# Performance work log

Hardware: AMD Instinct MI355X
Metric: run time of the kernel (lower is better)

Reference implementation:

```python
import jax, jax.numpy as jnp
import numpy as np

B, CH, H, W = 32, 128, 32, 32
EMB = 64      # embedding_dim
NEMB = 8192   # codebook size


def setup_inputs() -> dict:
    key = jax.random.key(0)
    k1, k2, k3, k4 = jax.random.split(key, 4)
    z = jax.random.normal(k1, (B, CH, H, W), jnp.float32)
    # 1x1 conv == per-pixel linear: weight [EMB, CH], bias [EMB]
    proj_w = jax.random.normal(k2, (EMB, CH), jnp.float32) * 0.05
    proj_b = jax.random.normal(k3, (EMB,), jnp.float32) * 0.01
    embed_w = jax.random.normal(k4, (NEMB, EMB), jnp.float32)
    return {"z": z, "proj_w": proj_w, "proj_b": proj_b, "embed_w": embed_w}


def reference(z, proj_w, proj_b, embed_w):
    Bz, C, Hh, Ww = z.shape
    sg = jax.lax.stop_gradient
    # 1x1 conv then permute(0,2,3,1): [B,C,H,W] -> [B,H,W,E]
    z_e = jnp.einsum('bchw,ec->bhwe', z, proj_w) + proj_b
    flat = z_e.reshape(-1, z_e.shape[-1])  # [N, E], N = B*H*W
    dist = ((flat * flat).sum(1, keepdims=True)
            - 2.0 * (flat @ embed_w.T)
            + (embed_w * embed_w).sum(1)[None, :])
    z_q_ind = jnp.argmin(dist, axis=1).reshape(Bz, Hh, Ww)  # argmax(-dist)
    z_q_emb = embed_w[z_q_ind]  # gather: [B,H,W,E]
    commitment_cost = 0.25
    kld_scale = 10.0
    latent_loss = kld_scale * (
        commitment_cost * jnp.mean((sg(z_q_emb) - z_e) ** 2)
        + jnp.mean((z_q_emb - sg(z_e)) ** 2))
    z_q_flat = z_q_emb
    # straight-through estimator
    z_q_st = z_e + sg(z_q_emb - z_e)
    out = jnp.transpose(z_q_st, (0, 3, 1, 2))  # [B,E,H,W]
    return out, z_q_flat, latent_loss, z_q_ind
```

## Files before the change

kernel.cpp:

```cpp
#include <hip/hip_runtime.h>

#define NPIX   32768
#define NEMB_  8192
#define EMB_   64
#define CH_    128
#define CAPP   768

#define OUT_OFF  0
#define ZQ_OFF   2097152
#define LOSS_OFF 4194304
#define IND_OFF  4194305

typedef _Float16 h8   __attribute__((ext_vector_type(8)));
typedef float    f16f __attribute__((ext_vector_type(16)));

__global__ __launch_bounds__(64) void k_wpack(
    const float* __restrict__ ew, const float* __restrict__ pw,
    float4* __restrict__ W4, float* __restrict__ pwT,
    float* __restrict__ wsq, float* __restrict__ wsqp,
    float* __restrict__ lacc, int* __restrict__ done)
{
    const int tid = threadIdx.x;
    {
        const int i = blockIdx.x * 64 + tid;
        const float v = pw[i];
        const int e = i >> 7, c = i & 127;
        pwT[c * 64 + e] = v;
    }
    const int m = blockIdx.x * 64 + tid;
    const float4* wr = (const float4*)(ew + (size_t)m * EMB_);
    float w[EMB_];
    float s = 0.f;
    #pragma unroll
    for (int i = 0; i < 16; i++) {
        float4 v = wr[i];
        w[4*i] = v.x; w[4*i+1] = v.y; w[4*i+2] = v.z; w[4*i+3] = v.w;
        s += v.x*v.x + v.y*v.y + v.z*v.z + v.w*v.w;
    }
    wsq[m] = s;
    float sh = (float)(_Float16)s;
    float sl = s - sh;
    const int t  = m >> 5;
    const int li = m & 31;
    #pragma unroll
    for (int s5 = 0; s5 < 4; s5++) {
        #pragma unroll
        for (int h = 0; h < 2; h++) {
            h8 hh;
            #pragma unroll
            for (int j = 0; j < 8; j++) hh[j] = (_Float16)w[s5 * 16 + h * 8 + j];
            W4[(size_t)(t * 5 + s5) * 64 + h * 32 + li] = __builtin_bit_cast(float4, hh);
        }
    }
    {
        h8 hh;
        #pragma unroll
        for (int j = 0; j < 8; j++) hh[j] = (_Float16)0.f;
        hh[0] = (_Float16)sh; hh[1] = (_Float16)sl;
        W4[(size_t)(t * 5 + 4) * 64 + 0 * 32 + li] = __builtin_bit_cast(float4, hh);
        #pragma unroll
        for (int j = 0; j < 8; j++) hh[j] = (_Float16)0.f;
        W4[(size_t)(t * 5 + 4) * 64 + 1 * 32 + li] = __builtin_bit_cast(float4, hh);
    }
    float sm = s;
    #pragma unroll
    for (int o = 32; o > 0; o >>= 1) sm = fmaxf(sm, __shfl_xor(sm, o));
    if (tid == 0) wsqp[blockIdx.x] = sm;
    if (blockIdx.x == 0 && tid == 0) { *lacc = 0.f; *done = 0; }
}

__device__ __forceinline__ unsigned long long pack_key(float d, int m)
{
    unsigned fb = __float_as_uint(d);
    fb ^= ((int)fb < 0) ? 0xFFFFFFFFu : 0x80000000u;
    return ((unsigned long long)fb << 32) | (unsigned)m;
}

__global__ __launch_bounds__(1024, 4) void k_fused3(
    const float4* __restrict__ W4, const float* __restrict__ z,
    const float* __restrict__ pwT, const float* __restrict__ pb,
    const float* __restrict__ wsqp, const float* __restrict__ wsq,
    const float* __restrict__ ew,
    float* __restrict__ out, float* __restrict__ lacc, int* __restrict__ done)
{
    __shared__ __align__(16) float xs[128][68];
    __shared__ float s1s[1024], s2s[1024], s3s[1024];
    __shared__ short i1s[1024], i2s[1024];
    __shared__ float xsqp_s[8][128];
    __shared__ float thr_s[128];
    __shared__ int   pairs[CAPP];
    __shared__ unsigned long long pbest[128];
    __shared__ int   winner_s[128];
    __shared__ int   smask[128];
    __shared__ float wred[16];
    __shared__ int   npair_s;
    __shared__ float wm_s;

    const int tid  = threadIdx.x;
    const int wv   = tid >> 6;
    const int lane = tid & 63;
    const int n0   = blockIdx.x * 128;
    const int hlf  = lane >> 5;

    if (tid == 0) npair_s = 0;
    if (tid < 128) { smask[tid] = 0; pbest[tid] = ~0ULL; }
    if (tid < 64) {
        float w = fmaxf(wsqp[tid], wsqp[tid + 64]);
        #pragma unroll
        for (int o = 32; o > 0; o >>= 1) w = fmaxf(w, __shfl_xor(w, o));
        if (tid == 0) wm_s = w;
    }

    {
        const int oct = tid >> 7;
        const int pxp = tid & 127;
        const int e0  = __builtin_amdgcn_readfirstlane(oct << 3);
        const float* zp = z + (size_t)(n0 >> 10) * (CH_ * 1024) + (n0 & 1023) + pxp;
        float acc[8];
        #pragma unroll
        for (int j = 0; j < 8; j++) acc[j] = 0.f;
        #pragma unroll 8
        for (int c = 0; c < CH_; c++) {
            const float zv = zp[(size_t)c * 1024];
            const float4* wr = (const float4*)(pwT + c * 64 + e0);
            float4 w0 = wr[0], w1 = wr[1];
            acc[0] = fmaf(zv, w0.x, acc[0]); acc[1] = fmaf(zv, w0.y, acc[1]);
            acc[2] = fmaf(zv, w0.z, acc[2]); acc[3] = fmaf(zv, w0.w, acc[3]);
            acc[4] = fmaf(zv, w1.x, acc[4]); acc[5] = fmaf(zv, w1.y, acc[5]);
            acc[6] = fmaf(zv, w1.z, acc[6]); acc[7] = fmaf(zv, w1.w, acc[7]);
        }
        const float4* pb4 = (const float4*)(pb + e0);
        float4 b0 = pb4[0], b1 = pb4[1];
        acc[0] += b0.x; acc[1] += b0.y; acc[2] += b0.z; acc[3] += b0.w;
        acc[4] += b1.x; acc[5] += b1.y; acc[6] += b1.z; acc[7] += b1.w;
        float sq = 0.f;
        #pragma unroll
        for (int j = 0; j < 8; j++) sq += acc[j] * acc[j];
        ((float4*)&xs[pxp][0])[oct * 2]     = make_float4(acc[0], acc[1], acc[2], acc[3]);
        ((float4*)&xs[pxp][0])[oct * 2 + 1] = make_float4(acc[4], acc[5], acc[6], acc[7]);
        xsqp_s[oct][pxp] = sq;
    }
    __syncthreads();

    const int ch = wv & 7;
    const int pg = wv >> 3;

    h8 bfr[2][4];
    #pragma unroll
    for (int j = 0; j < 2; j++) {
        const int px = pg * 64 + j * 32 + (lane & 31);
        #pragma unroll
        for (int s5 = 0; s5 < 4; s5++) {
            float4 u0 = *(const float4*)(&xs[px][s5 * 16 + hlf * 8]);
            float4 u1 = *(const float4*)(&xs[px][s5 * 16 + hlf * 8 + 4]);
            h8 hh;
            hh[0]=(_Float16)u0.x; hh[1]=(_Float16)u0.y; hh[2]=(_Float16)u0.z; hh[3]=(_Float16)u0.w;
            hh[4]=(_Float16)u1.x; hh[5]=(_Float16)u1.y; hh[6]=(_Float16)u1.z; hh[7]=(_Float16)u1.w;
            bfr[j][s5] = hh;
        }
    }
    h8 btail;
    {
        h8 hh;
        #pragma unroll
        for (int q = 0; q < 8; q++) hh[q] = (_Float16)0.f;
        if (hlf == 0) { hh[0] = (_Float16)-0.5f; hh[1] = (_Float16)-0.5f; }
        btail = hh;
    }

    const f16f kzero = {0,0,0,0,0,0,0,0,0,0,0,0,0,0,0,0};
    float s1[2], s2[2], s3[2];
    int   i1[2], i2[2];
    #pragma unroll
    for (int j = 0; j < 2; j++) { s1[j]=s2[j]=s3[j]=-3.0e38f; i1[j]=i2[j]=0; }

    const int tb = ch * 32;
    const float4* Wb = W4 + (size_t)tb * 320 + lane;
    float4 A[5];
    #pragma unroll
    for (int s = 0; s < 5; s++) A[s] = Wb[s * 64];

#define REDUCE_J(ACC, JJ, GT)                                                  \
    {                                                                          \
        float t0 = fmaxf(fmaxf(ACC[0],  ACC[1]),  ACC[2]);                     \
        float t1 = fmaxf(fmaxf(ACC[3],  ACC[4]),  ACC[5]);                     \
        float t2 = fmaxf(fmaxf(ACC[6],  ACC[7]),  ACC[8]);                     \
        float t3 = fmaxf(fmaxf(ACC[9],  ACC[10]), ACC[11]);                    \
        float t4 = fmaxf(fmaxf(ACC[12], ACC[13]), ACC[14]);                    \
        float v  = fmaxf(fmaxf(fmaxf(t0, t1), fmaxf(t2, t3)),                  \
                         fmaxf(t4, ACC[15]));                                  \
        bool c1 = v > s1[JJ];                                                  \
        bool c2 = v > s2[JJ];                                                  \
        int  cand = c1 ? i1[JJ] : (GT);                                        \
        i2[JJ] = c2 ? cand : i2[JJ];                                           \
        s3[JJ] = fmaxf(fminf(s2[JJ], v), s3[JJ]);                              \
        s3[JJ] = fminf(s3[JJ], fmaxf(s2[JJ], v));                              \
        s2[JJ] = fmaxf(fminf(s1[JJ], v), fminf(s2[JJ], fmaxf(s1[JJ], v)));     \
        i1[JJ] = c1 ? (GT) : i1[JJ];                                           \
        s1[JJ] = fmaxf(s1[JJ], v);                                             \
    }

    for (int tt = 0; tt < 32; tt++) {
        const int gt = tb + tt;
        f16f acc0 = __builtin_amdgcn_mfma_f32_32x32x16_f16(
            __builtin_bit_cast(h8, A[0]), bfr[0][0], kzero, 0, 0, 0);
        #pragma unroll
        for (int s = 1; s < 4; s++)
            acc0 = __builtin_amdgcn_mfma_f32_32x32x16_f16(
                __builtin_bit_cast(h8, A[s]), bfr[0][s], acc0, 0, 0, 0);
        acc0 = __builtin_amdgcn_mfma_f32_32x32x16_f16(
            __builtin_bit_cast(h8, A[4]), btail, acc0, 0, 0, 0);
        REDUCE_J(acc0, 0, gt)
        f16f acc1 = __builtin_amdgcn_mfma_f32_32x32x16_f16(
            __builtin_bit_cast(h8, A[0]), bfr[1][0], kzero, 0, 0, 0);
        #pragma unroll
        for (int s = 1; s < 4; s++)
            acc1 = __builtin_amdgcn_mfma_f32_32x32x16_f16(
                __builtin_bit_cast(h8, A[s]), bfr[1][s], acc1, 0, 0, 0);
        acc1 = __builtin_amdgcn_mfma_f32_32x32x16_f16(
            __builtin_bit_cast(h8, A[4]), btail, acc1, 0, 0, 0);
        {
            const int tp = (tt + 1) < 32 ? (tt + 1) : 31;
            const float4* wp = Wb + (size_t)tp * 320;
            #pragma unroll
            for (int s = 0; s < 5; s++) A[s] = wp[s * 64];
        }
        REDUCE_J(acc1, 1, gt)
    }
#undef REDUCE_J

    #pragma unroll
    for (int j = 0; j < 2; j++) {
        const float o1 = __shfl_xor(s1[j], 32);
        const float o2 = __shfl_xor(s2[j], 32);
        const float o3 = __shfl_xor(s3[j], 32);
        const int  oi1 = __shfl_xor(i1[j], 32);
        const int  oi2 = __shfl_xor(i2[j], 32);
        const bool a1  = s1[j] >= o1;
        const float m1 = a1 ? s1[j] : o1;
        const int  mi1 = a1 ? i1[j] : oi1;
        const float hA = a1 ? s2[j] : s1[j];
        const int  hAi = a1 ? i2[j] : i1[j];
        const float hB = a1 ? o1 : o2;
        const int  hBi = a1 ? oi1 : oi2;
        const bool b2  = hA >= hB;
        const float m2 = b2 ? hA : hB;
        const int  mi2 = b2 ? hAi : hBi;
        const float nA = b2 ? (a1 ? s3[j] : s2[j]) : hA;
        const float nB = b2 ? hB : (a1 ? o2 : o3);
        const float m3 = fmaxf(nA, nB);
        s1[j] = m1; s2[j] = m2; s3[j] = m3; i1[j] = mi1; i2[j] = mi2;
    }

    if (lane < 32) {
        #pragma unroll
        for (int j = 0; j < 2; j++) {
            const int px = pg * 64 + j * 32 + lane;
            const int cell = px * 8 + ch;
            s1s[cell] = s1[j]; s2s[cell] = s2[j]; s3s[cell] = s3[j];
            i1s[cell] = (short)i1[j]; i2s[cell] = (short)i2[j];
        }
    }
    __syncthreads();

    if (tid < 128) {
        float s1g = s1s[tid * 8];
        #pragma unroll
        for (int c = 1; c < 8; c++) s1g = fmaxf(s1g, s1s[tid * 8 + c]);
        float xq = xsqp_s[0][tid];
        #pragma unroll
        for (int o = 1; o < 8; o++) xq += xsqp_s[o][tid];
        float E = 0.00125f * sqrtf(xq * wm_s) + 1e-5f * wm_s + 3e-4f;
        thr_s[tid] = s1g - 2.0f * E;
    }
    __syncthreads();
    {
        const int cell = tid;
        const int px = cell >> 3, chh = cell & 7;
        const float th = thr_s[px];
        const float cs1 = s1s[cell], cs2 = s2s[cell], cs3 = s3s[cell];
        if (cs3 >= th) {
            int pos = atomicAdd(&npair_s, 32);
            if (pos + 32 <= CAPP) {
                for (int t = 0; t < 32; t++)
                    pairs[pos + t] = (px << 8) | (chh * 32 + t);
            } else {
                for (int t = 0; t < 32; t++)
                    if (pos + t < CAPP) pairs[pos + t] = -1;
                smask[px] = 1;
            }
        } else {
            if (cs1 >= th) {
                int pos = atomicAdd(&npair_s, 1);
                if (pos < CAPP) pairs[pos] = (px << 8) | (int)i1s[cell];
                else smask[px] = 1;
            }
            if (cs2 >= th) {
                int pos = atomicAdd(&npair_s, 1);
                if (pos < CAPP) pairs[pos] = (px << 8) | (int)i2s[cell];
                else smask[px] = 1;
            }
        }
    }
    __syncthreads();
    const int np = npair_s < CAPP ? npair_s : CAPP;

    const int lg = lane >> 4;
    const int ld = lane & 15;
    for (int i = wv; i < np; i += 16) {
        const int pr = pairs[i];
        if (pr < 0) continue;
        const int p = pr >> 8;
        if (smask[p]) continue;
        const int t = pr & 255;
        const float4* tb4 = (const float4*)(ew + (size_t)t * 2048);
        float4 wq[8];
        #pragma unroll
        for (int q = 0; q < 8; q++) wq[q] = tb4[q * 64 + lane];
        const float4 xq = *(const float4*)(&xs[p][ld * 4]);
        unsigned long long best = ~0ULL;
        #pragma unroll
        for (int q = 0; q < 8; q++) {
            float dp = wq[q].x*xq.x + wq[q].y*xq.y + wq[q].z*xq.z + wq[q].w*xq.w;
            dp += __shfl_xor(dp, 1);
            dp += __shfl_xor(dp, 2);
            dp += __shfl_xor(dp, 4);
            dp += __shfl_xor(dp, 8);
            const int m = t * 32 + q * 4 + lg;
            unsigned long long key = pack_key(fmaf(-2.f, dp, wsq[m]), m);
            best = key < best ? key : best;
        }
        { unsigned long long o = __shfl_xor(best, 16); best = o < best ? o : best; }
        { unsigned long long o = __shfl_xor(best, 32); best = o < best ? o : best; }
        if (lane == 0) atomicMin(&pbest[p], best);
    }
    for (int p = wv; p < 128; p += 16) {
        if (!smask[p]) continue;
        const float4 xq = *(const float4*)(&xs[p][ld * 4]);
        unsigned long long bk = ~0ULL;
        for (int t = 0; t < 256; t++) {
            const float4* tb4 = (const float4*)(ew + (size_t)t * 2048);
            #pragma unroll
            for (int q = 0; q < 8; q++) {
                float4 wv4 = tb4[q * 64 + lane];
                float dp = wv4.x*xq.x + wv4.y*xq.y + wv4.z*xq.z + wv4.w*xq.w;
                dp += __shfl_xor(dp, 1);
                dp += __shfl_xor(dp, 2);
                dp += __shfl_xor(dp, 4);
                dp += __shfl_xor(dp, 8);
                const int m = t * 32 + q * 4 + lg;
                unsigned long long key = pack_key(fmaf(-2.f, dp, wsq[m]), m);
                bk = key < bk ? key : bk;
            }
        }
        { unsigned long long o = __shfl_xor(bk, 16); bk = o < bk ? o : bk; }
        { unsigned long long o = __shfl_xor(bk, 32); bk = o < bk ? o : bk; }
        if (lane == 0) atomicMin(&pbest[p], bk);
    }
    __syncthreads();
    if (tid < 128) {
        const int win = (int)(unsigned)(pbest[tid] & 0xFFFFFFFFULL);
        winner_s[tid] = win;
        out[IND_OFF + n0 + tid] = (float)win;
    }
    __syncthreads();
    float lsum = 0.f;
    {
        const int px = tid >> 3, sg = tid & 7;
        const int win = winner_s[px];
        const float4* wr = (const float4*)(ew + (size_t)win * EMB_ + sg * 8);
        float4* xr  = (float4*)(&xs[px][sg * 8]);
        float4* zq4 = (float4*)(out + ZQ_OFF + (size_t)(n0 + px) * EMB_ + sg * 8);
        #pragma unroll
        for (int i = 0; i < 2; i++) {
            float4 w4v = wr[i];
            float4 z4  = xr[i];
            float d0 = w4v.x - z4.x, d1 = w4v.y - z4.y;
            float d2 = w4v.z - z4.z, d3 = w4v.w - z4.w;
            lsum += d0*d0 + d1*d1 + d2*d2 + d3*d3;
            xr[i]  = w4v;
            zq4[i] = w4v;
        }
    }
    __syncthreads();
    {
        const int bI  = n0 >> 10;
        const int hw0 = n0 & 1023;
        float* ob = out + OUT_OFF + (size_t)bI * (EMB_ * 1024) + hw0;
        #pragma unroll
        for (int r = 0; r < 8; r++) {
            const int idx = r * 1024 + tid;
            const int e = idx >> 7, px = idx & 127;
            ob[(size_t)e * 1024 + px] = xs[px][e];
        }
    }
    {
        float v = lsum;
        #pragma unroll
        for (int o = 1; o < 64; o <<= 1) v += __shfl_xor(v, o);
        if (lane == 0) wred[wv] = v;
    }
    __syncthreads();
    if (tid == 0) {
        float s = wred[0];
        #pragma unroll
        for (int k = 1; k < 16; k++) s += wred[k];
        atomicAdd(lacc, s);
        __threadfence();
        int old = atomicAdd(done, 1);
        if (old == (int)gridDim.x - 1) {
            float tot = atomicAdd(lacc, 0.0f);
            out[LOSS_OFF] = 12.5f * (tot / 2097152.0f);
        }
    }
}

extern "C" void kernel_launch(void* const* d_in, const int* in_sizes, int n_in,
                              void* d_out, int out_size, void* d_ws, size_t ws_size,
                              hipStream_t stream)
{
    const float* z  = (const float*)d_in[0];
    const float* pw = (const float*)d_in[1];
    const float* pb = (const float*)d_in[2];
    const float* ew = (const float*)d_in[3];
    float* out = (float*)d_out;

    char* ws = (char*)d_ws;
    float4* W4   = (float4*)(ws);
    float*  pwT  = (float*) (ws + 1310720);
    float*  wsq  = (float*) (ws + 1343488);
    float*  wsqp = (float*) (ws + 1376256);
    float*  lacc = (float*) (ws + 1376768);
    int*    done = (int*)   (ws + 1376772);

    hipLaunchKernelGGL(k_wpack,  dim3(128), dim3(64), 0, stream,
                       ew, pw, W4, pwT, wsq, wsqp, lacc, done);
    hipLaunchKernelGGL(k_fused3, dim3(256), dim3(1024), 0, stream,
                       W4, z, pwT, pb, wsqp, wsq, ew, out, lacc, done);
}
```

Measured before the change: 154.6 us.

## Stage codebook tiles into LDS with double-buffered global_load_lds shared across waves

Each codebook tile used by the distance MFMA loop is now copied into dynamic shared memory with async global-to-LDS loads. Only the first pixel-group waves issue the copy, and both pixel groups read the tile from LDS. The aim is to halve redundant global/L2 reads of the packed codebook and overlap the next tile's load with the current tile's compute. In exchange it adds a block-wide barrier every iteration across 16 waves, extra LDS reads, and 80 KB of dynamic shared memory, which may limit occupancy.

```diff
diff --git a/kernel.cpp b/kernel.cpp
--- a/kernel.cpp
+++ b/kernel.cpp
@@ -95,6 +95,7 @@
     __shared__ float wred[16];
     __shared__ int   npair_s;
     __shared__ float wm_s;
+    extern __shared__ __align__(16) float4 At[];
 
     const int tid  = threadIdx.x;
     const int wv   = tid >> 6;
@@ -144,6 +145,21 @@
 
     const int ch = wv & 7;
     const int pg = wv >> 3;
+    const int tb = ch * 32;
+
+#define STAGE(TILE, BUF)                                                       \
+    {                                                                          \
+        const float4* gs = W4 + (size_t)(tb + (TILE)) * 320 + lane;            \
+        float4* ls = &At[(size_t)((BUF) * 8 + ch) * 320];                      \
+        _Pragma("unroll")                                                      \
+        for (int s = 0; s < 5; s++)                                            \
+            __builtin_amdgcn_global_load_lds(                                  \
+                (const __attribute__((address_space(1))) void*)(gs + s * 64),  \
+                (__attribute__((address_space(3))) void*)(ls + s * 64),        \
+                16, 0, 0);                                                     \
+    }
+
+    if (pg == 0) STAGE(0, 0)
 
     h8 bfr[2][4];
     #pragma unroll
@@ -167,18 +183,13 @@
         if (hlf == 0) { hh[0] = (_Float16)-0.5f; hh[1] = (_Float16)-0.5f; }
         btail = hh;
     }
+    __syncthreads();
 
     const f16f kzero = {0,0,0,0,0,0,0,0,0,0,0,0,0,0,0,0};
     float s1[2], s2[2], s3[2];
     int   i1[2], i2[2];
     #pragma unroll
     for (int j = 0; j < 2; j++) { s1[j]=s2[j]=s3[j]=-3.0e38f; i1[j]=i2[j]=0; }
-
-    const int tb = ch * 32;
-    const float4* Wb = W4 + (size_t)tb * 320 + lane;
-    float4 A[5];
-    #pragma unroll
-    for (int s = 0; s < 5; s++) A[s] = Wb[s * 64];
 
 #define REDUCE_J(ACC, JJ, GT)                                                  \
     {                                                                          \
@@ -200,7 +211,13 @@
         s1[JJ] = fmaxf(s1[JJ], v);                                             \
     }
 
+    int buf = 0;
     for (int tt = 0; tt < 32; tt++) {
+        if (pg == 0 && (tt + 1) < 32) STAGE(tt + 1, buf ^ 1)
+        const float4* Ab = &At[(size_t)(buf * 8 + ch) * 320];
+        float4 A[5];
+        #pragma unroll
+        for (int s = 0; s < 5; s++) A[s] = Ab[s * 64 + lane];
         const int gt = tb + tt;
         f16f acc0 = __builtin_amdgcn_mfma_f32_32x32x16_f16(
             __builtin_bit_cast(h8, A[0]), bfr[0][0], kzero, 0, 0, 0);
@@ -219,15 +236,12 @@
                 __builtin_bit_cast(h8, A[s]), bfr[1][s], acc1, 0, 0, 0);
         acc1 = __builtin_amdgcn_mfma_f32_32x32x16_f16(
             __builtin_bit_cast(h8, A[4]), btail, acc1, 0, 0, 0);
-        {
-            const int tp = (tt + 1) < 32 ? (tt + 1) : 31;
-            const float4* wp = Wb + (size_t)tp * 320;
-            #pragma unroll
-            for (int s = 0; s < 5; s++) A[s] = wp[s * 64];
-        }
         REDUCE_J(acc1, 1, gt)
+        __syncthreads();
+        buf ^= 1;
     }
 #undef REDUCE_J
+#undef STAGE
 
     #pragma unroll
     for (int j = 0; j < 2; j++) {
@@ -433,8 +447,16 @@
     float*  lacc = (float*) (ws + 1376768);
     int*    done = (int*)   (ws + 1376772);
 
+    static bool attr_set = false;
+    if (!attr_set) {
+        (void)hipFuncSetAttribute((const void*)k_fused3,
+                                  hipFuncAttributeMaxDynamicSharedMemorySize,
+                                  81920);
+        attr_set = true;
+    }
+
     hipLaunchKernelGGL(k_wpack,  dim3(128), dim3(64), 0, stream,
                        ew, pw, W4, pwT, wsq, wsqp, lacc, done);
-    hipLaunchKernelGGL(k_fused3, dim3(256), dim3(1024), 0, stream,
+    hipLaunchKernelGGL(k_fused3, dim3(256), dim3(1024), 81920, stream,
                        W4, z, pwT, pb, wsqp, wsq, ew, out, lacc, done);
 }
```

New measurement: 160.2 us. +3.6%, slower.
